# Optimization experiments

Measured on AMD Instinct MI355X. Metric: run time of the kernel, lower is better.

The kernel has to match this reference:

```python
import jax, jax.numpy as jnp
from jax import lax
import numpy as np

B, H, W = 4, 512, 512
CIN, COUT, BASE, NL = 3, 3, 64, 4
EPS = 1e-5


def _conv(x, w, b, stride=1, pad=0):
    y = lax.conv_general_dilated(x, w, (stride, stride), ((pad, pad), (pad, pad)),
                                 dimension_numbers=('NCHW', 'OIHW', 'NCHW'))
    return y + b[None, :, None, None]


def _convT(x, w, b):
    # torch ConvTranspose2d(k=3, stride=2, padding=1, output_padding=1); w is [Cin, Cout, 3, 3]
    w_ = jnp.flip(w, (2, 3)).transpose(1, 0, 2, 3)  # -> OIHW
    k = w.shape[2]
    lo, hi = k - 1 - 1, k - 1 - 1 + 1  # (1, 2): pad=1, output_padding=1
    y = lax.conv_general_dilated(x, w_, (1, 1), ((lo, hi), (lo, hi)), lhs_dilation=(2, 2),
                                 dimension_numbers=('NCHW', 'OIHW', 'NCHW'))
    return y + b[None, :, None, None]


def _inorm(x):
    m = x.mean((2, 3), keepdims=True)
    v = x.var((2, 3), keepdims=True)  # biased, matches torch InstanceNorm2d
    return (x - m) * lax.rsqrt(v + EPS)


def _refl(x, p=3):
    return jnp.pad(x, ((0, 0), (0, 0), (p, p), (p, p)), mode='reflect')


def setup_inputs() -> dict:
    key = jax.random.key(0)
    ks = jax.random.split(key, 16)
    s = 0.05
    inp = {}
    inp['x'] = jax.random.normal(ks[0], (B, CIN, H, W), jnp.float32)
    inp['inst'] = jax.random.randint(ks[1], (B, 1, H, W), 0, 10)
    inp['w0'] = jax.random.normal(ks[2], (BASE, CIN, 7, 7), jnp.float32) * s
    inp['b0'] = jnp.zeros((BASE,), jnp.float32)
    c, ki = BASE, 3
    for i in range(NL):
        inp[f'dw{i}'] = jax.random.normal(ks[ki], (2 * c, c, 3, 3), jnp.float32) * s
        inp[f'db{i}'] = jnp.zeros((2 * c,), jnp.float32)
        c *= 2; ki += 1
    for i in range(NL):
        inp[f'uw{i}'] = jax.random.normal(ks[ki], (c, c // 2, 3, 3), jnp.float32) * s  # torch ConvT layout [Cin,Cout,k,k]
        inp[f'ub{i}'] = jnp.zeros((c // 2,), jnp.float32)
        c //= 2; ki += 1
    inp['wf'] = jax.random.normal(ks[ki], (COUT, BASE, 7, 7), jnp.float32) * s
    inp['bf'] = jnp.zeros((COUT,), jnp.float32)
    return inp


def reference(x, w0, b0, dw0, db0, dw1, db1, dw2, db2, dw3, db3,
              uw0, ub0, uw1, ub1, uw2, ub2, uw3, ub3, wf, bf, inst):
    h = jax.nn.relu(_inorm(_conv(_refl(x), w0, b0)))
    for w_, b_ in ((dw0, db0), (dw1, db1), (dw2, db2), (dw3, db3)):
        h = jax.nn.relu(_inorm(_conv(h, w_, b_, stride=2, pad=1)))
    for w_, b_ in ((uw0, ub0), (uw1, ub1), (uw2, ub2), (uw3, ub3)):
        h = jax.nn.relu(_inorm(_convT(h, w_, b_)))
    h = jnp.tanh(_conv(_refl(h), wf, bf))
    # instancewise_average_pooling: original loops classes but always masks inst==1,
    # so the result is the per-(batch, channel) mean over inst==1 pixels scattered
    # back onto those pixels, zeros elsewhere.
    mask = (inst == 1).astype(h.dtype)            # [B,1,H,W]
    cnt = mask.sum((2, 3))                        # [B,1]
    mean = (h * mask).sum((2, 3)) / cnt           # [B,C]
    return mean[:, :, None, None] * mask
```

## Files before the change

kernel.cpp:

```cpp
#include <hip/hip_runtime.h>
#include <math.h>


typedef _Float16 half_t;
typedef _Float16 halfx8 __attribute__((ext_vector_type(8)));
typedef _Float16 halfx4 __attribute__((ext_vector_type(4)));
typedef float floatx4 __attribute__((ext_vector_type(4)));

static __device__ __forceinline__ float xform(float v, float m, float r) {
  v = (v - m) * r;
  return v > 0.f ? v : 0.f;
}

__global__ __launch_bounds__(256) void transform_w(
    const float* __restrict__ src, half_t* __restrict__ dst,
    int Cin, int Cout, int mode)
{
  int idx = blockIdx.x * 256 + threadIdx.x;
  int total = Cin * Cout * 9;
  if (idx >= total) return;
  int tap = idx % 9, t2 = idx / 9;
  int co, ci;
  if (mode == 0) { ci = t2 % Cin; co = t2 / Cin; }
  else           { co = t2 % Cout; ci = t2 / Cout; }
  dst[((size_t)tap * Cout + co) * Cin + ci] = (half_t)src[idx];
}

__global__ __launch_bounds__(256) void transform_wf(
    const float* __restrict__ src, half_t* __restrict__ dst)
{
  int idx = blockIdx.x * 256 + threadIdx.x;
  if (idx >= 49 * 16 * 64) return;
  int ci = idx & 63, t = idx >> 6;
  int co = t & 15, tap = t >> 4;
  float v = (co < 3) ? src[((size_t)co * 64 + ci) * 49 + tap] : 0.f;
  dst[idx] = (half_t)v;
}

__global__ __launch_bounds__(256) void transform_w0(
    const float* __restrict__ src, half_t* __restrict__ dst)
{
  int idx = blockIdx.x * 256 + threadIdx.x;
  if (idx >= 7 * 64 * 32) return;
  int k = idx & 31, t = idx >> 5;
  int co = t & 63, ky = t >> 6;
  int kx = k >> 2, ci = k & 3;
  float v = (ci < 3 && kx < 7) ? src[(((size_t)co * 3 + ci) * 7 + ky) * 7 + kx] : 0.f;
  dst[idx] = (half_t)v;
}

__global__ __launch_bounds__(256) void conv0_mfma(
    const float* __restrict__ x, const half_t* __restrict__ wt,
    const float* __restrict__ bias, half_t* __restrict__ out)
{
  const int H = 512, W = 512;
  __shared__ _Float16 sX[22 * 24 * 4];
  __shared__ _Float16 sO[256 * 72];
  const int tile = blockIdx.x, b = blockIdx.y;
  const int tx0 = (tile & 31) << 4, ty0 = (tile >> 5) << 4;
  const int tid = threadIdx.x;
  const int wave = tid >> 6, lane = tid & 63;
  const int ln = lane & 15, g = lane >> 4;

  for (int u = tid; u < 22 * 24; u += 256) {
    int row = u / 24, col = u % 24;
    halfx4 v = {0, 0, 0, 0};
    if (col < 22) {
      int gy = ty0 + row - 3, gx = tx0 + col - 3;
      gy = gy < 0 ? -gy : (gy >= H ? 2 * H - 2 - gy : gy);
      gx = gx < 0 ? -gx : (gx >= W ? 2 * W - 2 - gx : gx);
      size_t p = (size_t)b * 3 * H * W + (size_t)gy * W + gx;
      v[0] = (_Float16)x[p];
      v[1] = (_Float16)x[p + H * W];
      v[2] = (_Float16)x[p + 2 * H * W];
    }
    *(halfx4*)(&sX[u * 4]) = v;
  }
  __syncthreads();

  floatx4 acc[4][4];
#pragma unroll
  for (int r = 0; r < 4; ++r)
#pragma unroll
    for (int n = 0; n < 4; ++n) acc[r][n] = floatx4{0.f, 0.f, 0.f, 0.f};

#pragma unroll
  for (int ky = 0; ky < 7; ++ky) {
    halfx8 wb[4];
#pragma unroll
    for (int nt = 0; nt < 4; ++nt)
      wb[nt] = *(const halfx8*)(wt + ((size_t)ky * 64 + nt * 16 + ln) * 32 + g * 8);
#pragma unroll
    for (int rr = 0; rr < 4; ++rr) {
      int y = wave * 4 + rr;
      halfx8 a = *(const halfx8*)(&sX[((y + ky) * 24 + ln + 2 * g) * 4]);
#pragma unroll
      for (int nt = 0; nt < 4; ++nt)
        acc[rr][nt] = __builtin_amdgcn_mfma_f32_16x16x32_f16(a, wb[nt], acc[rr][nt], 0, 0, 0);
    }
  }

  float bs[4];
#pragma unroll
  for (int nt = 0; nt < 4; ++nt) bs[nt] = bias[nt * 16 + ln];
#pragma unroll
  for (int rr = 0; rr < 4; ++rr)
#pragma unroll
    for (int nt = 0; nt < 4; ++nt)
#pragma unroll
      for (int i = 0; i < 4; ++i) {
        int p = (wave * 4 + rr) * 16 + g * 4 + i;
        sO[p * 72 + nt * 16 + ln] = (half_t)(acc[rr][nt][i] + bs[nt]);
      }
  __syncthreads();
  {
    int p = tid;
    int oy = ty0 + (p >> 4), ox = tx0 + (p & 15);
    size_t ob = ((size_t)(b * 512 + oy) * 512 + ox) * 64;
#pragma unroll
    for (int j = 0; j < 8; ++j)
      *(halfx8*)(&out[ob + j * 8]) = *(const halfx8*)(&sO[p * 72 + j * 8]);
  }
}

__global__ __launch_bounds__(256) void stats_part(
    const half_t* __restrict__ x, float* __restrict__ Ssum, int C, int S)
{
  const int b = blockIdx.y, tid = threadIdx.x;
  const size_t base = (size_t)b * S * C;
  const int E8 = (S * C) >> 3;
  float s[8], s2[8];
#pragma unroll
  for (int j = 0; j < 8; ++j) { s[j] = 0.f; s2[j] = 0.f; }
  for (int i8 = blockIdx.x * 256 + tid; i8 < E8; i8 += gridDim.x * 256) {
    halfx8 v = *(const halfx8*)(x + base + (size_t)i8 * 8);
#pragma unroll
    for (int j = 0; j < 8; ++j) {
      float f = (float)v[j];
      s[j] += f; s2[j] += f * f;
    }
  }
  __shared__ float part[256][16];
#pragma unroll
  for (int j = 0; j < 8; ++j) { part[tid][j] = s[j]; part[tid][8 + j] = s2[j]; }
  __syncthreads();
  const int T = C >> 3, reps = 256 / (C >> 3);
  for (int c = tid; c < C; c += 256) {
    int r = c >> 3, j = c & 7;
    float ss = 0.f, ss2 = 0.f;
    for (int m = 0; m < reps; ++m) {
      ss += part[r + m * T][j];
      ss2 += part[r + m * T][8 + j];
    }
    atomicAdd(&Ssum[(size_t)(b * C + c) * 2], ss);
    atomicAdd(&Ssum[(size_t)(b * C + c) * 2 + 1], ss2);
  }
}

__global__ __launch_bounds__(256) void finalize_stats(
    const float* __restrict__ Ssum, float* __restrict__ mean,
    float* __restrict__ rstd, int total, float invN)
{
  int idx = blockIdx.x * 256 + threadIdx.x;
  if (idx >= total) return;
  float sm = Ssum[(size_t)idx * 2], s2 = Ssum[(size_t)idx * 2 + 1];
  float m = sm * invN;
  float var = s2 * invN - m * m;
  mean[idx] = m;
  rstd[idx] = rsqrtf(var + 1e-5f);
}

__global__ __launch_bounds__(256) void down_mfma(
    const half_t* __restrict__ in, const half_t* __restrict__ wt,
    const float* __restrict__ bias, const float* __restrict__ mean,
    const float* __restrict__ rstd, half_t* __restrict__ out,
    int Cin, int Cout, int IH, int IW)
{
  const int OH = IH >> 1, OW = IW >> 1;
  __shared__ _Float16 sX[9 * 33 * 40];
  const int tid = threadIdx.x;
  const int wave = tid >> 6, lane = tid & 63;
  const int ln = lane & 15, g = lane >> 4;
  const int cog = blockIdx.x, b = blockIdx.z;
  const int ntx = OW >> 4;
  const int ox0 = (blockIdx.y % ntx) << 4, oy0 = (blockIdx.y / ntx) << 2;
  const int iy0 = 2 * oy0 - 1, ix0 = 2 * ox0 - 1;
  const int coW = cog * 128 + wave * 32;
  const int q = tid & 3;

  floatx4 acc[4][2];
#pragma unroll
  for (int r = 0; r < 4; ++r)
#pragma unroll
    for (int n = 0; n < 2; ++n) acc[r][n] = floatx4{0.f, 0.f, 0.f, 0.f};

  for (int c0 = 0; c0 < Cin; c0 += 32) {
    float mq[8], rq[8];
#pragma unroll
    for (int j = 0; j < 8; ++j) {
      int cc = c0 + q * 8 + j;
      mq[j] = mean[b * Cin + cc];
      rq[j] = rstd[b * Cin + cc];
    }
    __syncthreads();
    for (int idx = tid; idx < 9 * 33 * 4; idx += 256) {
      int p = idx >> 2;
      int y = p / 33, xx = p % 33;
      int gy = iy0 + y, gx = ix0 + xx;
      halfx8 v = {0, 0, 0, 0, 0, 0, 0, 0};
      if ((unsigned)gy < (unsigned)IH && (unsigned)gx < (unsigned)IW) {
        v = *(const halfx8*)(in + ((size_t)(b * IH + gy) * IW + gx) * Cin + c0 + q * 8);
#pragma unroll
        for (int j = 0; j < 8; ++j) {
          float f = ((float)v[j] - mq[j]) * rq[j];
          v[j] = (_Float16)(f > 0.f ? f : 0.f);
        }
      }
      *(halfx8*)(&sX[(y * 33 + xx) * 40 + q * 8]) = v;
    }
    __syncthreads();
#pragma unroll
    for (int tap = 0; tap < 9; ++tap) {
      const int ky = tap / 3, kx = tap % 3;
      halfx8 wb0 = *(const halfx8*)(wt + ((size_t)tap * Cout + coW + ln) * Cin + c0 + g * 8);
      halfx8 wb1 = *(const halfx8*)(wt + ((size_t)tap * Cout + coW + 16 + ln) * Cin + c0 + g * 8);
#pragma unroll
      for (int r = 0; r < 4; ++r) {
        halfx8 a = *(const halfx8*)(&sX[((2 * r + ky) * 33 + 2 * ln + kx) * 40 + g * 8]);
        acc[r][0] = __builtin_amdgcn_mfma_f32_16x16x32_f16(a, wb0, acc[r][0], 0, 0, 0);
        acc[r][1] = __builtin_amdgcn_mfma_f32_16x16x32_f16(a, wb1, acc[r][1], 0, 0, 0);
      }
    }
  }
#pragma unroll
  for (int nt = 0; nt < 2; ++nt) {
    int co = coW + nt * 16 + ln;
    float bs = bias[co];
#pragma unroll
    for (int r = 0; r < 4; ++r)
#pragma unroll
      for (int i = 0; i < 4; ++i) {
        int oy = oy0 + r, ox = ox0 + g * 4 + i;
        out[((size_t)(b * OH + oy) * OW + ox) * Cout + co] = (half_t)(acc[r][nt][i] + bs);
      }
  }
}

__global__ __launch_bounds__(256) void up_mfma(
    const half_t* __restrict__ in, const half_t* __restrict__ wt,
    const float* __restrict__ bias, const float* __restrict__ mean,
    const float* __restrict__ rstd, half_t* __restrict__ out,
    int Cin, int Cout, int IH, int IW)
{
  const int OH = IH << 1, OW = IW << 1;
  __shared__ _Float16 sX[5 * 17 * 40];
  const int tid = threadIdx.x;
  const int wave = tid >> 6, lane = tid & 63;
  const int ln = lane & 15, g = lane >> 4;
  const int cog = blockIdx.x, b = blockIdx.z;
  const int ntx = OW >> 5;
  const int ox0 = (blockIdx.y % ntx) << 5, oy0 = (blockIdx.y / ntx) << 3;
  const int iyb = oy0 >> 1, ixb = ox0 >> 1;
  const int co = cog * 64 + wave * 16 + ln;
  const int q = tid & 3;

  floatx4 acc[4][4];
#pragma unroll
  for (int c = 0; c < 4; ++c)
#pragma unroll
    for (int r = 0; r < 4; ++r) acc[c][r] = floatx4{0.f, 0.f, 0.f, 0.f};

  for (int c0 = 0; c0 < Cin; c0 += 32) {
    float mq[8], rq[8];
#pragma unroll
    for (int j = 0; j < 8; ++j) {
      int cc = c0 + q * 8 + j;
      mq[j] = mean[b * Cin + cc];
      rq[j] = rstd[b * Cin + cc];
    }
    __syncthreads();
    for (int idx = tid; idx < 5 * 17 * 4; idx += 256) {
      int p = idx >> 2;
      int y = p / 17, xx = p % 17;
      int gy = iyb + y, gx = ixb + xx;
      halfx8 v = {0, 0, 0, 0, 0, 0, 0, 0};
      if (gy < IH && gx < IW) {
        v = *(const halfx8*)(in + ((size_t)(b * IH + gy) * IW + gx) * Cin + c0 + q * 8);
#pragma unroll
        for (int j = 0; j < 8; ++j) {
          float f = ((float)v[j] - mq[j]) * rq[j];
          v[j] = (_Float16)(f > 0.f ? f : 0.f);
        }
      }
      *(halfx8*)(&sX[(y * 17 + xx) * 40 + q * 8]) = v;
    }
    __syncthreads();
#pragma unroll
    for (int tap = 0; tap < 9; ++tap) {
      const int ky = tap / 3, kx = tap % 3;
      const int cls = ((ky == 1) ? 0 : 2) + ((kx == 1) ? 0 : 1);
      const int dy = (ky == 0) ? 1 : 0;
      const int dx = (kx == 0) ? 1 : 0;
      halfx8 wb = *(const halfx8*)(wt + ((size_t)tap * Cout + co) * Cin + c0 + g * 8);
#pragma unroll
      for (int r = 0; r < 4; ++r) {
        halfx8 a = *(const halfx8*)(&sX[((r + dy) * 17 + ln + dx) * 40 + g * 8]);
        acc[cls][r] = __builtin_amdgcn_mfma_f32_16x16x32_f16(a, wb, acc[cls][r], 0, 0, 0);
      }
    }
  }
  float bs = bias[co];
#pragma unroll
  for (int cls = 0; cls < 4; ++cls) {
    const int ey = cls >> 1, ex = cls & 1;
#pragma unroll
    for (int r = 0; r < 4; ++r)
#pragma unroll
      for (int i = 0; i < 4; ++i) {
        int oy = oy0 + 2 * r + ey;
        int ox = ox0 + 2 * (g * 4 + i) + ex;
        out[((size_t)(b * OH + oy) * OW + ox) * Cout + co] = (half_t)(acc[cls][r][i] + bs);
      }
  }
}

__global__ __launch_bounds__(256) void convf_mfma(
    const half_t* __restrict__ in, const half_t* __restrict__ wt,
    const float* __restrict__ bias, const float* __restrict__ mean,
    const float* __restrict__ rstd, float* __restrict__ out)
{
  const int H = 512, W = 512;
  __shared__ _Float16 sX[22 * 22 * 72];
  const int tile = blockIdx.x, b = blockIdx.y;
  const int tx0 = (tile & 31) << 4, ty0 = (tile >> 5) << 4;
  const int tid = threadIdx.x;
  const int wave = tid >> 6, lane = tid & 63;
  const int ln = lane & 15, g = lane >> 4;
  const int oct = tid & 7;

  float mq[8], rq[8];
#pragma unroll
  for (int j = 0; j < 8; ++j) {
    mq[j] = mean[b * 64 + oct * 8 + j];
    rq[j] = rstd[b * 64 + oct * 8 + j];
  }
  for (int u = tid; u < 484 * 8; u += 256) {
    int p = u >> 3;
    int iy = p / 22, ix = p % 22;
    int gy = ty0 + iy - 3, gx = tx0 + ix - 3;
    gy = gy < 0 ? -gy : (gy >= H ? 2 * H - 2 - gy : gy);
    gx = gx < 0 ? -gx : (gx >= W ? 2 * W - 2 - gx : gx);
    halfx8 v = *(const halfx8*)(in + ((size_t)(b * H + gy) * W + gx) * 64 + oct * 8);
#pragma unroll
    for (int j = 0; j < 8; ++j) {
      float f = ((float)v[j] - mq[j]) * rq[j];
      v[j] = (_Float16)(f > 0.f ? f : 0.f);
    }
    *(halfx8*)(&sX[p * 72 + oct * 8]) = v;
  }
  __syncthreads();

  floatx4 acc[4];
#pragma unroll
  for (int r = 0; r < 4; ++r) acc[r] = floatx4{0.f, 0.f, 0.f, 0.f};

  for (int tap = 0; tap < 49; ++tap) {
    const int ky = tap / 7, kx = tap % 7;
#pragma unroll
    for (int kc = 0; kc < 2; ++kc) {
      halfx8 wb = *(const halfx8*)(wt + ((size_t)tap * 16 + ln) * 64 + kc * 32 + g * 8);
#pragma unroll
      for (int rr = 0; rr < 4; ++rr) {
        int y = wave * 4 + rr;
        halfx8 a = *(const halfx8*)(&sX[((y + ky) * 22 + ln + kx) * 72 + kc * 32 + g * 8]);
        acc[rr] = __builtin_amdgcn_mfma_f32_16x16x32_f16(a, wb, acc[rr], 0, 0, 0);
      }
    }
  }
  if (ln < 3) {
    float bs = bias[ln];
#pragma unroll
    for (int rr = 0; rr < 4; ++rr) {
      int oy = ty0 + wave * 4 + rr;
#pragma unroll
      for (int i = 0; i < 4; ++i) {
        int ox = tx0 + g * 4 + i;
        out[((size_t)(b * 3 + ln) * H + oy) * W + ox] = tanhf(acc[rr][i] + bs);
      }
    }
  }
}

__global__ __launch_bounds__(256) void pool_sum_kernel(
    const float* __restrict__ f, const int* __restrict__ inst,
    float* __restrict__ P)
{
  const int N = 512 * 512;
  const int b = blockIdx.x, chunk = blockIdx.y;
  const int per = N / 32;
  const int base = chunk * per;
  float s0 = 0.f, s1 = 0.f, s2 = 0.f, c = 0.f;
  for (int i = base + threadIdx.x; i < base + per; i += 256) {
    if (inst[b * N + i] == 1) {
      c += 1.f;
      s0 += f[(size_t)(b * 3 + 0) * N + i];
      s1 += f[(size_t)(b * 3 + 1) * N + i];
      s2 += f[(size_t)(b * 3 + 2) * N + i];
    }
  }
#pragma unroll
  for (int off = 32; off > 0; off >>= 1) {
    s0 += __shfl_down(s0, off); s1 += __shfl_down(s1, off);
    s2 += __shfl_down(s2, off); c += __shfl_down(c, off);
  }
  __shared__ float red[4][4];
  int wv = threadIdx.x >> 6;
  if ((threadIdx.x & 63) == 0) {
    red[wv][0] = s0; red[wv][1] = s1; red[wv][2] = s2; red[wv][3] = c;
  }
  __syncthreads();
  if (threadIdx.x == 0) {
    float t0 = red[0][0] + red[1][0] + red[2][0] + red[3][0];
    float t1 = red[0][1] + red[1][1] + red[2][1] + red[3][1];
    float t2 = red[0][2] + red[1][2] + red[2][2] + red[3][2];
    float tc = red[0][3] + red[1][3] + red[2][3] + red[3][3];
    atomicAdd(&P[b * 4 + 0], t0);
    atomicAdd(&P[b * 4 + 1], t1);
    atomicAdd(&P[b * 4 + 2], t2);
    atomicAdd(&P[b * 4 + 3], tc);
  }
}

__global__ __launch_bounds__(256) void pool_scatter_kernel(
    const int* __restrict__ inst, const float* __restrict__ P,
    float* __restrict__ out)
{
  const int N = 512 * 512;
  int idx = blockIdx.x * 256 + threadIdx.x;
  if (idx >= 4 * N) return;
  int b = idx >> 18;
  int i = idx & (N - 1);
  bool m = inst[idx] == 1;
  float inv = 1.f / P[b * 4 + 3];
  out[(size_t)(b * 3 + 0) * N + i] = m ? P[b * 4 + 0] * inv : 0.f;
  out[(size_t)(b * 3 + 1) * N + i] = m ? P[b * 4 + 1] * inv : 0.f;
  out[(size_t)(b * 3 + 2) * N + i] = m ? P[b * 4 + 2] * inv : 0.f;
}

extern "C" void kernel_launch(void* const* d_in, const int* in_sizes, int n_in,
                              void* d_out, int out_size, void* d_ws, size_t ws_size,
                              hipStream_t stream)
{
  (void)in_sizes; (void)n_in; (void)out_size; (void)ws_size;
  const float* x    = (const float*)d_in[0];
  const int*   inst = (const int*)d_in[1];
  const float* w0   = (const float*)d_in[2];
  const float* b0   = (const float*)d_in[3];
  const float *dw[4], *db[4], *uw[4], *ub[4];
  for (int i = 0; i < 4; ++i) {
    dw[i] = (const float*)d_in[4 + 2 * i];
    db[i] = (const float*)d_in[5 + 2 * i];
    uw[i] = (const float*)d_in[12 + 2 * i];
    ub[i] = (const float*)d_in[13 + 2 * i];
  }
  const float* wf = (const float*)d_in[20];
  const float* bf = (const float*)d_in[21];

  char* base = (char*)d_ws;
  half_t* A  = (half_t*)base;
  half_t* Bh = (half_t*)(base + 134217728);
  float*  F  = (float*)(base + 134217728);
  float*  Ssum   = (float*)(base + 201326592);
  float*  S_mean = (float*)(base + 201326592 + 32768);
  float*  S_rstd = (float*)(base + 201326592 + 49152);
  float*  P      = (float*)(base + 201326592 + 65536);
  half_t* WTp0   = (half_t*)(base + 201326592 + 66560);
  half_t* WTp1   = (half_t*)(base + 201326592 + 66560 + 147456);
  half_t* WTf    = (half_t*)(base + 201326592 + 66560 + 294912);
  half_t* WT0    = (half_t*)(base + 201326592 + 66560 + 294912 + 100352);
  half_t* WTA    = (half_t*)(base + 124780544);
  half_t* WTB    = (half_t*)(base + 191889408);

  auto XFORM = [&](const float* src, half_t* dst, int Ci, int Co, int mode) {
    int tot = Ci * Co * 9;
    transform_w<<<dim3((tot + 255) / 256), 256, 0, stream>>>(src, dst, Ci, Co, mode);
  };
  auto STATS = [&](const half_t* p, int C, int S) {
    hipMemsetAsync(Ssum, 0, 4096 * 2 * sizeof(float), stream);
    stats_part<<<dim3(128, 4), 256, 0, stream>>>(p, Ssum, C, S);
    finalize_stats<<<dim3((4 * C + 255) / 256), 256, 0, stream>>>(
        Ssum, S_mean, S_rstd, 4 * C, 1.f / (float)S);
  };

  transform_w0<<<dim3((7 * 64 * 32 + 255) / 256), 256, 0, stream>>>(w0, WT0);
  transform_wf<<<dim3((49 * 16 * 64 + 255) / 256), 256, 0, stream>>>(wf, WTf);
  conv0_mfma<<<dim3(1024, 4), 256, 0, stream>>>(x, WT0, b0, A);
  STATS(A, 64, 512 * 512);

  XFORM(dw[0], WTp0, 64, 128, 0);
  down_mfma<<<dim3(1, 1024, 4), 256, 0, stream>>>(A, WTp0, db[0], S_mean, S_rstd, Bh, 64, 128, 512, 512);
  STATS(Bh, 128, 256 * 256);
  XFORM(dw[1], WTA, 128, 256, 0);
  down_mfma<<<dim3(2, 256, 4), 256, 0, stream>>>(Bh, WTA, db[1], S_mean, S_rstd, A, 128, 256, 256, 256);
  STATS(A, 256, 128 * 128);
  XFORM(dw[2], WTB, 256, 512, 0);
  down_mfma<<<dim3(4, 64, 4), 256, 0, stream>>>(A, WTB, db[2], S_mean, S_rstd, Bh, 256, 512, 128, 128);
  STATS(Bh, 512, 64 * 64);
  XFORM(dw[3], WTA, 512, 1024, 0);
  down_mfma<<<dim3(8, 16, 4), 256, 0, stream>>>(Bh, WTA, db[3], S_mean, S_rstd, A, 512, 1024, 64, 64);
  STATS(A, 1024, 32 * 32);

  XFORM(uw[0], WTB, 1024, 512, 1);
  up_mfma<<<dim3(8, 16, 4), 256, 0, stream>>>(A, WTB, ub[0], S_mean, S_rstd, Bh, 1024, 512, 32, 32);
  STATS(Bh, 512, 64 * 64);
  XFORM(uw[1], WTA, 512, 256, 1);
  up_mfma<<<dim3(4, 64, 4), 256, 0, stream>>>(Bh, WTA, ub[1], S_mean, S_rstd, A, 512, 256, 64, 64);
  STATS(A, 256, 128 * 128);
  XFORM(uw[2], WTA, 256, 128, 1);
  up_mfma<<<dim3(2, 256, 4), 256, 0, stream>>>(A, WTA, ub[2], S_mean, S_rstd, Bh, 256, 128, 128, 128);
  STATS(Bh, 128, 256 * 256);
  XFORM(uw[3], WTp1, 128, 64, 1);
  up_mfma<<<dim3(1, 1024, 4), 256, 0, stream>>>(Bh, WTp1, ub[3], S_mean, S_rstd, A, 128, 64, 256, 256);
  STATS(A, 64, 512 * 512);

  convf_mfma<<<dim3(1024, 4), 256, 0, stream>>>(A, WTf, bf, S_mean, S_rstd, F);
  hipMemsetAsync(P, 0, 16 * sizeof(float), stream);
  pool_sum_kernel<<<dim3(4, 32), 256, 0, stream>>>(F, inst, P);
  pool_scatter_kernel<<<dim3(4096), 256, 0, stream>>>(inst, P, (float*)d_out);
}
```

Before: 1.591 ms.

## Fuse instance-norm statistics into conv epilogues and drop separate stats passes

Each conv kernel now accumulates per-channel sum and sum-of-squares in its epilogue, using wave shuffles and global atomics. Consumers compute mean and rstd inline from these sums, so the separate stats_part and finalize_stats kernels and their per-layer memsets go away, saving a full read of every activation tensor. convf also stages input channels in two 32-channel chunks to shrink its shared-memory footprint. In exchange it adds many atomics, which makes the float sums non-deterministic, and changes the LDS reuse pattern in convf.

```diff
diff --git a/kernel.cpp b/kernel.cpp
--- a/kernel.cpp
+++ b/kernel.cpp
@@ -6,11 +6,6 @@
 typedef _Float16 halfx8 __attribute__((ext_vector_type(8)));
 typedef _Float16 halfx4 __attribute__((ext_vector_type(4)));
 typedef float floatx4 __attribute__((ext_vector_type(4)));
-
-static __device__ __forceinline__ float xform(float v, float m, float r) {
-  v = (v - m) * r;
-  return v > 0.f ? v : 0.f;
-}
 
 __global__ __launch_bounds__(256) void transform_w(
     const float* __restrict__ src, half_t* __restrict__ dst,
@@ -51,7 +46,8 @@
 
 __global__ __launch_bounds__(256) void conv0_mfma(
     const float* __restrict__ x, const half_t* __restrict__ wt,
-    const float* __restrict__ bias, half_t* __restrict__ out)
+    const float* __restrict__ bias, half_t* __restrict__ out,
+    float* __restrict__ ssOut)
 {
   const int H = 512, W = 512;
   __shared__ _Float16 sX[22 * 24 * 4];
@@ -100,18 +96,26 @@
     }
   }
 
-  float bs[4];
-#pragma unroll
-  for (int nt = 0; nt < 4; ++nt) bs[nt] = bias[nt * 16 + ln];
-#pragma unroll
-  for (int rr = 0; rr < 4; ++rr)
-#pragma unroll
-    for (int nt = 0; nt < 4; ++nt)
+#pragma unroll
+  for (int nt = 0; nt < 4; ++nt) {
+    float bs = bias[nt * 16 + ln];
+    float s = 0.f, s2 = 0.f;
+#pragma unroll
+    for (int rr = 0; rr < 4; ++rr)
 #pragma unroll
       for (int i = 0; i < 4; ++i) {
         int p = (wave * 4 + rr) * 16 + g * 4 + i;
-        sO[p * 72 + nt * 16 + ln] = (half_t)(acc[rr][nt][i] + bs[nt]);
-      }
+        float v = acc[rr][nt][i] + bs;
+        s += v; s2 += v * v;
+        sO[p * 72 + nt * 16 + ln] = (half_t)v;
+      }
+    s += __shfl_xor(s, 16); s += __shfl_xor(s, 32);
+    s2 += __shfl_xor(s2, 16); s2 += __shfl_xor(s2, 32);
+    if (g == 0) {
+      atomicAdd(&ssOut[(size_t)(b * 64 + nt * 16 + ln) * 2], s);
+      atomicAdd(&ssOut[(size_t)(b * 64 + nt * 16 + ln) * 2 + 1], s2);
+    }
+  }
   __syncthreads();
   {
     int p = tid;
@@ -123,57 +127,10 @@
   }
 }
 
-__global__ __launch_bounds__(256) void stats_part(
-    const half_t* __restrict__ x, float* __restrict__ Ssum, int C, int S)
-{
-  const int b = blockIdx.y, tid = threadIdx.x;
-  const size_t base = (size_t)b * S * C;
-  const int E8 = (S * C) >> 3;
-  float s[8], s2[8];
-#pragma unroll
-  for (int j = 0; j < 8; ++j) { s[j] = 0.f; s2[j] = 0.f; }
-  for (int i8 = blockIdx.x * 256 + tid; i8 < E8; i8 += gridDim.x * 256) {
-    halfx8 v = *(const halfx8*)(x + base + (size_t)i8 * 8);
-#pragma unroll
-    for (int j = 0; j < 8; ++j) {
-      float f = (float)v[j];
-      s[j] += f; s2[j] += f * f;
-    }
-  }
-  __shared__ float part[256][16];
-#pragma unroll
-  for (int j = 0; j < 8; ++j) { part[tid][j] = s[j]; part[tid][8 + j] = s2[j]; }
-  __syncthreads();
-  const int T = C >> 3, reps = 256 / (C >> 3);
-  for (int c = tid; c < C; c += 256) {
-    int r = c >> 3, j = c & 7;
-    float ss = 0.f, ss2 = 0.f;
-    for (int m = 0; m < reps; ++m) {
-      ss += part[r + m * T][j];
-      ss2 += part[r + m * T][8 + j];
-    }
-    atomicAdd(&Ssum[(size_t)(b * C + c) * 2], ss);
-    atomicAdd(&Ssum[(size_t)(b * C + c) * 2 + 1], ss2);
-  }
-}
-
-__global__ __launch_bounds__(256) void finalize_stats(
-    const float* __restrict__ Ssum, float* __restrict__ mean,
-    float* __restrict__ rstd, int total, float invN)
-{
-  int idx = blockIdx.x * 256 + threadIdx.x;
-  if (idx >= total) return;
-  float sm = Ssum[(size_t)idx * 2], s2 = Ssum[(size_t)idx * 2 + 1];
-  float m = sm * invN;
-  float var = s2 * invN - m * m;
-  mean[idx] = m;
-  rstd[idx] = rsqrtf(var + 1e-5f);
-}
-
 __global__ __launch_bounds__(256) void down_mfma(
     const half_t* __restrict__ in, const half_t* __restrict__ wt,
-    const float* __restrict__ bias, const float* __restrict__ mean,
-    const float* __restrict__ rstd, half_t* __restrict__ out,
+    const float* __restrict__ bias, const float* __restrict__ ssIn,
+    float invN, half_t* __restrict__ out, float* __restrict__ ssOut,
     int Cin, int Cout, int IH, int IW)
 {
   const int OH = IH >> 1, OW = IW >> 1;
@@ -199,8 +156,11 @@
 #pragma unroll
     for (int j = 0; j < 8; ++j) {
       int cc = c0 + q * 8 + j;
-      mq[j] = mean[b * Cin + cc];
-      rq[j] = rstd[b * Cin + cc];
+      float sA = ssIn[(size_t)(b * Cin + cc) * 2];
+      float sB = ssIn[(size_t)(b * Cin + cc) * 2 + 1];
+      float m = sA * invN;
+      mq[j] = m;
+      rq[j] = rsqrtf(sB * invN - m * m + 1e-5f);
     }
     __syncthreads();
     for (int idx = tid; idx < 9 * 33 * 4; idx += 256) {
@@ -236,20 +196,29 @@
   for (int nt = 0; nt < 2; ++nt) {
     int co = coW + nt * 16 + ln;
     float bs = bias[co];
+    float s = 0.f, s2 = 0.f;
 #pragma unroll
     for (int r = 0; r < 4; ++r)
 #pragma unroll
       for (int i = 0; i < 4; ++i) {
         int oy = oy0 + r, ox = ox0 + g * 4 + i;
-        out[((size_t)(b * OH + oy) * OW + ox) * Cout + co] = (half_t)(acc[r][nt][i] + bs);
-      }
+        float v = acc[r][nt][i] + bs;
+        s += v; s2 += v * v;
+        out[((size_t)(b * OH + oy) * OW + ox) * Cout + co] = (half_t)v;
+      }
+    s += __shfl_xor(s, 16); s += __shfl_xor(s, 32);
+    s2 += __shfl_xor(s2, 16); s2 += __shfl_xor(s2, 32);
+    if (g == 0) {
+      atomicAdd(&ssOut[(size_t)(b * Cout + co) * 2], s);
+      atomicAdd(&ssOut[(size_t)(b * Cout + co) * 2 + 1], s2);
+    }
   }
 }
 
 __global__ __launch_bounds__(256) void up_mfma(
     const half_t* __restrict__ in, const half_t* __restrict__ wt,
-    const float* __restrict__ bias, const float* __restrict__ mean,
-    const float* __restrict__ rstd, half_t* __restrict__ out,
+    const float* __restrict__ bias, const float* __restrict__ ssIn,
+    float invN, half_t* __restrict__ out, float* __restrict__ ssOut,
     int Cin, int Cout, int IH, int IW)
 {
   const int OH = IH << 1, OW = IW << 1;
@@ -275,8 +244,11 @@
 #pragma unroll
     for (int j = 0; j < 8; ++j) {
       int cc = c0 + q * 8 + j;
-      mq[j] = mean[b * Cin + cc];
-      rq[j] = rstd[b * Cin + cc];
+      float sA = ssIn[(size_t)(b * Cin + cc) * 2];
+      float sB = ssIn[(size_t)(b * Cin + cc) * 2 + 1];
+      float m = sA * invN;
+      mq[j] = m;
+      rq[j] = rsqrtf(sB * invN - m * m + 1e-5f);
     }
     __syncthreads();
     for (int idx = tid; idx < 5 * 17 * 4; idx += 256) {
@@ -310,6 +282,7 @@
     }
   }
   float bs = bias[co];
+  float s = 0.f, s2 = 0.f;
 #pragma unroll
   for (int cls = 0; cls < 4; ++cls) {
     const int ey = cls >> 1, ex = cls & 1;
@@ -319,60 +292,71 @@
       for (int i = 0; i < 4; ++i) {
         int oy = oy0 + 2 * r + ey;
         int ox = ox0 + 2 * (g * 4 + i) + ex;
-        out[((size_t)(b * OH + oy) * OW + ox) * Cout + co] = (half_t)(acc[cls][r][i] + bs);
-      }
+        float v = acc[cls][r][i] + bs;
+        s += v; s2 += v * v;
+        out[((size_t)(b * OH + oy) * OW + ox) * Cout + co] = (half_t)v;
+      }
+  }
+  s += __shfl_xor(s, 16); s += __shfl_xor(s, 32);
+  s2 += __shfl_xor(s2, 16); s2 += __shfl_xor(s2, 32);
+  if (g == 0) {
+    atomicAdd(&ssOut[(size_t)(b * Cout + co) * 2], s);
+    atomicAdd(&ssOut[(size_t)(b * Cout + co) * 2 + 1], s2);
   }
 }
 
 __global__ __launch_bounds__(256) void convf_mfma(
     const half_t* __restrict__ in, const half_t* __restrict__ wt,
-    const float* __restrict__ bias, const float* __restrict__ mean,
-    const float* __restrict__ rstd, float* __restrict__ out)
+    const float* __restrict__ bias, const float* __restrict__ ssIn,
+    float invN, float* __restrict__ out)
 {
   const int H = 512, W = 512;
-  __shared__ _Float16 sX[22 * 22 * 72];
+  __shared__ _Float16 sX[484 * 40];
   const int tile = blockIdx.x, b = blockIdx.y;
   const int tx0 = (tile & 31) << 4, ty0 = (tile >> 5) << 4;
   const int tid = threadIdx.x;
   const int wave = tid >> 6, lane = tid & 63;
   const int ln = lane & 15, g = lane >> 4;
-  const int oct = tid & 7;
-
-  float mq[8], rq[8];
-#pragma unroll
-  for (int j = 0; j < 8; ++j) {
-    mq[j] = mean[b * 64 + oct * 8 + j];
-    rq[j] = rstd[b * 64 + oct * 8 + j];
-  }
-  for (int u = tid; u < 484 * 8; u += 256) {
-    int p = u >> 3;
-    int iy = p / 22, ix = p % 22;
-    int gy = ty0 + iy - 3, gx = tx0 + ix - 3;
-    gy = gy < 0 ? -gy : (gy >= H ? 2 * H - 2 - gy : gy);
-    gx = gx < 0 ? -gx : (gx >= W ? 2 * W - 2 - gx : gx);
-    halfx8 v = *(const halfx8*)(in + ((size_t)(b * H + gy) * W + gx) * 64 + oct * 8);
+  const int oc = tid & 3;
+
+  floatx4 acc[4];
+#pragma unroll
+  for (int r = 0; r < 4; ++r) acc[r] = floatx4{0.f, 0.f, 0.f, 0.f};
+
+  for (int c0 = 0; c0 < 64; c0 += 32) {
+    float mq[8], rq[8];
 #pragma unroll
     for (int j = 0; j < 8; ++j) {
-      float f = ((float)v[j] - mq[j]) * rq[j];
-      v[j] = (_Float16)(f > 0.f ? f : 0.f);
-    }
-    *(halfx8*)(&sX[p * 72 + oct * 8]) = v;
-  }
-  __syncthreads();
-
-  floatx4 acc[4];
-#pragma unroll
-  for (int r = 0; r < 4; ++r) acc[r] = floatx4{0.f, 0.f, 0.f, 0.f};
-
-  for (int tap = 0; tap < 49; ++tap) {
-    const int ky = tap / 7, kx = tap % 7;
-#pragma unroll
-    for (int kc = 0; kc < 2; ++kc) {
-      halfx8 wb = *(const halfx8*)(wt + ((size_t)tap * 16 + ln) * 64 + kc * 32 + g * 8);
+      int cc = c0 + oc * 8 + j;
+      float sA = ssIn[(size_t)(b * 64 + cc) * 2];
+      float sB = ssIn[(size_t)(b * 64 + cc) * 2 + 1];
+      float m = sA * invN;
+      mq[j] = m;
+      rq[j] = rsqrtf(sB * invN - m * m + 1e-5f);
+    }
+    __syncthreads();
+    for (int u = tid; u < 484 * 4; u += 256) {
+      int p = u >> 2;
+      int iy = p / 22, ix = p % 22;
+      int gy = ty0 + iy - 3, gx = tx0 + ix - 3;
+      gy = gy < 0 ? -gy : (gy >= H ? 2 * H - 2 - gy : gy);
+      gx = gx < 0 ? -gx : (gx >= W ? 2 * W - 2 - gx : gx);
+      halfx8 v = *(const halfx8*)(in + ((size_t)(b * H + gy) * W + gx) * 64 + c0 + oc * 8);
+#pragma unroll
+      for (int j = 0; j < 8; ++j) {
+        float f = ((float)v[j] - mq[j]) * rq[j];
+        v[j] = (_Float16)(f > 0.f ? f : 0.f);
+      }
+      *(halfx8*)(&sX[p * 40 + oc * 8]) = v;
+    }
+    __syncthreads();
+    for (int tap = 0; tap < 49; ++tap) {
+      const int ky = tap / 7, kx = tap % 7;
+      halfx8 wb = *(const halfx8*)(wt + ((size_t)tap * 16 + ln) * 64 + c0 + g * 8);
 #pragma unroll
       for (int rr = 0; rr < 4; ++rr) {
         int y = wave * 4 + rr;
-        halfx8 a = *(const halfx8*)(&sX[((y + ky) * 22 + ln + kx) * 72 + kc * 32 + g * 8]);
+        halfx8 a = *(const halfx8*)(&sX[((y + ky) * 22 + ln + kx) * 40 + g * 8]);
         acc[rr] = __builtin_amdgcn_mfma_f32_16x16x32_f16(a, wb, acc[rr], 0, 0, 0);
       }
     }
@@ -470,61 +454,52 @@
   half_t* A  = (half_t*)base;
   half_t* Bh = (half_t*)(base + 134217728);
   float*  F  = (float*)(base + 134217728);
-  float*  Ssum   = (float*)(base + 201326592);
-  float*  S_mean = (float*)(base + 201326592 + 32768);
-  float*  S_rstd = (float*)(base + 201326592 + 49152);
-  float*  P      = (float*)(base + 201326592 + 65536);
-  half_t* WTp0   = (half_t*)(base + 201326592 + 66560);
-  half_t* WTp1   = (half_t*)(base + 201326592 + 66560 + 147456);
-  half_t* WTf    = (half_t*)(base + 201326592 + 66560 + 294912);
-  half_t* WT0    = (half_t*)(base + 201326592 + 66560 + 294912 + 100352);
-  half_t* WTA    = (half_t*)(base + 124780544);
-  half_t* WTB    = (half_t*)(base + 191889408);
+  float*  SS = (float*)(base + 201326592);
+  float*  P    = (float*)(base + 201326592 + 94208);
+  half_t* WTp0 = (half_t*)(base + 201326592 + 95232);
+  half_t* WTp1 = (half_t*)(base + 201326592 + 95232 + 147456);
+  half_t* WTf  = (half_t*)(base + 201326592 + 95232 + 294912);
+  half_t* WT0  = (half_t*)(base + 201326592 + 95232 + 294912 + 100352);
+  half_t* WTA  = (half_t*)(base + 124780544);
+  half_t* WTB  = (half_t*)(base + 191889408);
+
+  float* S0 = SS;          float* S1 = SS + 512;   float* S2 = SS + 1536;
+  float* S3 = SS + 3584;   float* S4 = SS + 7680;  float* S5 = SS + 15872;
+  float* S6 = SS + 19968;  float* S7 = SS + 22016; float* S8 = SS + 23040;
+  const float i512 = 1.f / (512.f * 512.f), i256 = 1.f / (256.f * 256.f),
+              i128 = 1.f / (128.f * 128.f), i64 = 1.f / (64.f * 64.f),
+              i32 = 1.f / (32.f * 32.f);
 
   auto XFORM = [&](const float* src, half_t* dst, int Ci, int Co, int mode) {
     int tot = Ci * Co * 9;
     transform_w<<<dim3((tot + 255) / 256), 256, 0, stream>>>(src, dst, Ci, Co, mode);
   };
-  auto STATS = [&](const half_t* p, int C, int S) {
-    hipMemsetAsync(Ssum, 0, 4096 * 2 * sizeof(float), stream);
-    stats_part<<<dim3(128, 4), 256, 0, stream>>>(p, Ssum, C, S);
-    finalize_stats<<<dim3((4 * C + 255) / 256), 256, 0, stream>>>(
-        Ssum, S_mean, S_rstd, 4 * C, 1.f / (float)S);
-  };
+
+  hipMemsetAsync(SS, 0, 94208 + 1024, stream);
 
   transform_w0<<<dim3((7 * 64 * 32 + 255) / 256), 256, 0, stream>>>(w0, WT0);
   transform_wf<<<dim3((49 * 16 * 64 + 255) / 256), 256, 0, stream>>>(wf, WTf);
-  conv0_mfma<<<dim3(1024, 4), 256, 0, stream>>>(x, WT0, b0, A);
-  STATS(A, 64, 512 * 512);
+  conv0_mfma<<<dim3(1024, 4), 256, 0, stream>>>(x, WT0, b0, A, S0);
 
   XFORM(dw[0], WTp0, 64, 128, 0);
-  down_mfma<<<dim3(1, 1024, 4), 256, 0, stream>>>(A, WTp0, db[0], S_mean, S_rstd, Bh, 64, 128, 512, 512);
-  STATS(Bh, 128, 256 * 256);
+  down_mfma<<<dim3(1, 1024, 4), 256, 0, stream>>>(A, WTp0, db[0], S0, i512, Bh, S1, 64, 128, 512, 512);
   XFORM(dw[1], WTA, 128, 256, 0);
-  down_mfma<<<dim3(2, 256, 4), 256, 0, stream>>>(Bh, WTA, db[1], S_mean, S_rstd, A, 128, 256, 256, 256);
-  STATS(A, 256, 128 * 128);
+  down_mfma<<<dim3(2, 256, 4), 256, 0, stream>>>(Bh, WTA, db[1], S1, i256, A, S2, 128, 256, 256, 256);
   XFORM(dw[2], WTB, 256, 512, 0);
-  down_mfma<<<dim3(4, 64, 4), 256, 0, stream>>>(A, WTB, db[2], S_mean, S_rstd, Bh, 256, 512, 128, 128);
-  STATS(Bh, 512, 64 * 64);
+  down_mfma<<<dim3(4, 64, 4), 256, 0, stream>>>(A, WTB, db[2], S2, i128, Bh, S3, 256, 512, 128, 128);
   XFORM(dw[3], WTA, 512, 1024, 0);
-  down_mfma<<<dim3(8, 16, 4), 256, 0, stream>>>(Bh, WTA, db[3], S_mean, S_rstd, A, 512, 1024, 64, 64);
-  STATS(A, 1024, 32 * 32);
+  down_mfma<<<dim3(8, 16, 4), 256, 0, stream>>>(Bh, WTA, db[3], S3, i64, A, S4, 512, 1024, 64, 64);
 
   XFORM(uw[0], WTB, 1024, 512, 1);
-  up_mfma<<<dim3(8, 16, 4), 256, 0, stream>>>(A, WTB, ub[0], S_mean, S_rstd, Bh, 1024, 512, 32, 32);
-  STATS(Bh, 512, 64 * 64);
+  up_mfma<<<dim3(8, 16, 4), 256, 0, stream>>>(A, WTB, ub[0], S4, i32, Bh, S5, 1024, 512, 32, 32);
   XFORM(uw[1], WTA, 512, 256, 1);
-  up_mfma<<<dim3(4, 64, 4), 256, 0, stream>>>(Bh, WTA, ub[1], S_mean, S_rstd, A, 512, 256, 64, 64);
-  STATS(A, 256, 128 * 128);
+  up_mfma<<<dim3(4, 64, 4), 256, 0, stream>>>(Bh, WTA, ub[1], S5, i64, A, S6, 512, 256, 64, 64);
   XFORM(uw[2], WTA, 256, 128, 1);
-  up_mfma<<<dim3(2, 256, 4), 256, 0, stream>>>(A, WTA, ub[2], S_mean, S_rstd, Bh, 256, 128, 128, 128);
-  STATS(Bh, 128, 256 * 256);
+  up_mfma<<<dim3(2, 256, 4), 256, 0, stream>>>(A, WTA, ub[2], S6, i128, Bh, S7, 256, 128, 128, 128);
   XFORM(uw[3], WTp1, 128, 64, 1);
-  up_mfma<<<dim3(1, 1024, 4), 256, 0, stream>>>(Bh, WTp1, ub[3], S_mean, S_rstd, A, 128, 64, 256, 256);
-  STATS(A, 64, 512 * 512);
-
-  convf_mfma<<<dim3(1024, 4), 256, 0, stream>>>(A, WTf, bf, S_mean, S_rstd, F);
-  hipMemsetAsync(P, 0, 16 * sizeof(float), stream);
+  up_mfma<<<dim3(1, 1024, 4), 256, 0, stream>>>(Bh, WTp1, ub[3], S7, i256, A, S8, 128, 64, 256, 256);
+
+  convf_mfma<<<dim3(1024, 4), 256, 0, stream>>>(A, WTf, bf, S8, i512, F);
   pool_sum_kernel<<<dim3(4, 32), 256, 0, stream>>>(F, inst, P);
   pool_scatter_kernel<<<dim3(4096), 256, 0, stream>>>(inst, P, (float*)d_out);
 }
```

Result: slower. 2.079 ms (+30.7%).
